# Kernel tuning notes

Hardware: AMD Instinct MI355X
Metric: run time of the kernel (lower is better)

The kernel has to match this reference:

```python
import jax, jax.numpy as jnp
import numpy as np

B, T, D, H = 128, 256, 1024, 1024


def setup_inputs() -> dict:
    key = jax.random.key(0)
    ks = jax.random.split(key, 6)
    s = 0.02
    return {
        "x": jax.random.normal(ks[0], (B, T, D), dtype=jnp.float32),
        "mask": jnp.ones((B, T), dtype=jnp.float32),
        "Wi_f": jax.random.normal(ks[1], (3 * H, D), dtype=jnp.float32) * s,
        "Wh_f": jax.random.normal(ks[2], (3 * H, H), dtype=jnp.float32) * s,
        "bi_f": jnp.zeros((3 * H,), dtype=jnp.float32),
        "bh_f": jnp.zeros((3 * H,), dtype=jnp.float32),
        "Wi_r": jax.random.normal(ks[3], (3 * H, D), dtype=jnp.float32) * s,
        "Wh_r": jax.random.normal(ks[4], (3 * H, H), dtype=jnp.float32) * s,
        "bi_r": jnp.zeros((3 * H,), dtype=jnp.float32),
        "bh_r": jnp.zeros((3 * H,), dtype=jnp.float32),
    }


def _gru_scan(x_tbd, m_tb, Wi, Wh, bi, bh):
    # x_tbd: [T,B,D], m_tb: [T,B]; returns all hidden states [T,B,H]
    h0 = jnp.zeros((x_tbd.shape[1], Wh.shape[1]), dtype=x_tbd.dtype)

    def step(h, inp):
        x_t, m_t = inp
        gi = x_t @ Wi.T + bi          # [B,3H]
        gh = h @ Wh.T + bh            # [B,3H]
        i_r, i_z, i_n = jnp.split(gi, 3, axis=-1)
        h_r, h_z, h_n = jnp.split(gh, 3, axis=-1)
        r = jax.nn.sigmoid(i_r + h_r)
        z = jax.nn.sigmoid(i_z + h_z)
        n = jnp.tanh(i_n + r * h_n)
        h_new = (1.0 - z) * n + z * h
        m = m_t[:, None]
        h_out = m * h_new + (1.0 - m) * h  # masked carry-over
        return h_out, h_out

    _, hs = jax.lax.scan(step, h0, (x_tbd, m_tb))
    return hs


def reference(x, mask, Wi_f, Wh_f, bi_f, bh_f, Wi_r, Wh_r, bi_r, bh_r):
    x_t = jnp.transpose(x, (1, 0, 2))   # [T,B,D]
    m_t = jnp.transpose(mask, (1, 0))   # [T,B]
    hs_f = _gru_scan(x_t, m_t, Wi_f, Wh_f, bi_f, bh_f)              # forward in time
    hs_r = _gru_scan(x_t[::-1], m_t[::-1], Wi_r, Wh_r, bi_r, bh_r)  # reverse in time
    hs_r = hs_r[::-1]
    out = jnp.concatenate([hs_f, hs_r], axis=-1)  # [T,B,2H]
    return jnp.transpose(out, (1, 0, 2))          # [B,T,2H]
```

## Files before the change

kernel.cpp:

```cpp
#include <hip/hip_runtime.h>
#include <hip/hip_bf16.h>

typedef __hip_bfloat16 bf16;
typedef __attribute__((ext_vector_type(8))) short bf16x8;
typedef __attribute__((ext_vector_type(4))) float f32x4;

#define GLDS16(g, l)                                                  \
  __builtin_amdgcn_global_load_lds(                                   \
      (const __attribute__((address_space(1))) void*)(g),             \
      (__attribute__((address_space(3))) void*)(l), 16, 0, 0)

__device__ __forceinline__ float bf2f(bf16 v) { return __bfloat162float(v); }
__device__ __forceinline__ short f2bf(float f) {
  bf16 b = __float2bfloat16(f);
  return *reinterpret_cast<short*>(&b);
}

__device__ __forceinline__ unsigned long long ald64(const void* p) {
  return __hip_atomic_load((const unsigned long long*)p, __ATOMIC_RELAXED,
                           __HIP_MEMORY_SCOPE_AGENT);
}
__device__ __forceinline__ void ast32(void* p, unsigned v) {
  __hip_atomic_store((unsigned*)p, v, __ATOMIC_RELAXED,
                     __HIP_MEMORY_SCOPE_AGENT);
}
__device__ __forceinline__ unsigned ald32(const void* p) {
  return __hip_atomic_load((const unsigned*)p, __ATOMIC_RELAXED,
                           __HIP_MEMORY_SCOPE_AGENT);
}

__global__ __launch_bounds__(256) void cvt_bf16(const float* __restrict__ in,
                                                bf16* __restrict__ out, int n) {
  const int i = (blockIdx.x * 256 + threadIdx.x) * 8;
  if (i >= n) return;
  const float4 u = *(const float4*)(in + i);
  const float4 v = *(const float4*)(in + i + 4);
  bf16x8 w;
  w[0] = f2bf(u.x); w[1] = f2bf(u.y); w[2] = f2bf(u.z); w[3] = f2bf(u.w);
  w[4] = f2bf(v.x); w[5] = f2bf(v.y); w[6] = f2bf(v.z); w[7] = f2bf(v.w);
  *(bf16x8*)(out + i) = w;
}

__global__ __launch_bounds__(256) void cvt_whb(const float* __restrict__ Wh_f,
                                               const float* __restrict__ Wh_r,
                                               bf16* __restrict__ Whb) {
  const int t = blockIdx.x * 256 + threadIdx.x;
  const int d = t / 393216;
  int r = t % 393216;
  const int cg = r / 6144;  r %= 6144;
  const int g = r / 2048;   r %= 2048;
  const int kk = r / 64;
  const int lane = r & 63;
  const float* Wh = d ? Wh_r : Wh_f;
  const int row = g * 1024 + cg * 16 + (lane & 15);
  const int col = kk * 32 + (lane >> 4) * 8;
  const float* s = Wh + (size_t)row * 1024 + col;
  const float4 u = *(const float4*)s;
  const float4 v = *(const float4*)(s + 4);
  bf16x8 w;
  w[0] = f2bf(u.x); w[1] = f2bf(u.y); w[2] = f2bf(u.z); w[3] = f2bf(u.w);
  w[4] = f2bf(v.x); w[5] = f2bf(v.y); w[6] = f2bf(v.z); w[7] = f2bf(v.w);
  *(bf16x8*)(Whb + (size_t)t * 8) = w;
}

__global__ __launch_bounds__(256) void gi_gemm(const bf16* __restrict__ X,
                                               const bf16* __restrict__ Wi,
                                               const float* __restrict__ bi,
                                               bf16* __restrict__ Gi) {
  __shared__ bf16 As[128 * 32];
  __shared__ bf16 Bs[128 * 32];
  const int tid = threadIdx.x;
  const int lane = tid & 63;
  const int w = tid >> 6;
  const int wm = w >> 1, wn = w & 1;
  const int m0 = blockIdx.y * 128;
  const int n0 = blockIdx.x * 128;
  const int rA = lane & 15;
  const int kl = (lane >> 4) * 8;

  f32x4 acc[4][4] = {};

  const bf16* Ab = X + (size_t)m0 * 1024;
  const bf16* Bb = Wi + (size_t)n0 * 1024;

  const int arow = tid >> 2;
  const int akk = (tid & 3) * 8;

  for (int kt = 0; kt < 1024; kt += 32) {
#pragma unroll
    for (int i = 0; i < 2; ++i) {
      GLDS16(Ab + (size_t)(i * 64 + arow) * 1024 + kt + akk,
             As + (i * 256 + w * 64) * 8);
      GLDS16(Bb + (size_t)(i * 64 + arow) * 1024 + kt + akk,
             Bs + (i * 256 + w * 64) * 8);
    }
    asm volatile("s_waitcnt vmcnt(0)" ::: "memory");
    __syncthreads();

    bf16x8 a[4], b[4];
#pragma unroll
    for (int f = 0; f < 4; ++f) {
      a[f] = *(const bf16x8*)(As + (wm * 64 + f * 16 + rA) * 32 + kl);
      b[f] = *(const bf16x8*)(Bs + (wn * 64 + f * 16 + rA) * 32 + kl);
    }
#pragma unroll
    for (int mf = 0; mf < 4; ++mf)
#pragma unroll
      for (int nf = 0; nf < 4; ++nf)
        acc[mf][nf] = __builtin_amdgcn_mfma_f32_16x16x32_bf16(
            a[mf], b[nf], acc[mf][nf], 0, 0, 0);
    __syncthreads();
  }

  const int rgrp = (lane >> 4) * 4;
#pragma unroll
  for (int nf = 0; nf < 4; ++nf) {
    const int col = n0 + wn * 64 + nf * 16 + rA;
    const float bv = bi[col];
#pragma unroll
    for (int mf = 0; mf < 4; ++mf) {
#pragma unroll
      for (int j = 0; j < 4; ++j) {
        const int row = m0 + wm * 64 + mf * 16 + rgrp + j;
        Gi[(size_t)row * 3072 + col] = __float2bfloat16(acc[mf][nf][j] + bv);
      }
    }
  }
}

__global__ __launch_bounds__(128, 1) void gru_persist_f(
    const bf16* __restrict__ Whb, const float* __restrict__ bh_f,
    const float* __restrict__ bh_r, const bf16* __restrict__ Gi,
    const float* __restrict__ mask, bf16* __restrict__ h16,
    unsigned* __restrict__ flags, float* __restrict__ out) {
  __shared__ bf16 hs[32 * 1024];
  const int tid = threadIdx.x;
  const int lane = tid & 63;
  const int w = tid >> 6;
  const int mg = w;
  const int bid = blockIdx.x;
  const int chain = bid & 7;
  const int ct = bid >> 3;
  const int dir = chain >> 2;
  const int bt = chain & 3;
  unsigned* gflags = flags + chain * 128;

  const float* bh = dir ? bh_r : bh_f;
  const bf16* gi = Gi + (size_t)dir * (32768ull * 3072ull);
  const int bt0 = bt * 32;
  const int rA = lane & 15;
  const int klane = lane >> 4;
  const int row = mg * 16 + rA;
  const int colg = ct * 16 + rA;

  bf16* hbuf0 = h16 + (size_t)(dir * 2 + 0) * 131072;
  bf16* hbuf1 = h16 + (size_t)(dir * 2 + 1) * 131072;

  const bf16* bp = Whb + (size_t)dir * 3145728 + (size_t)(ct * 3) * 16384 +
                   lane * 8;
  bf16x8 br[32], bz[32];
#pragma unroll
  for (int kk = 0; kk < 32; ++kk) br[kk] = *(const bf16x8*)(bp + kk * 512);
#pragma unroll
  for (int kk = 0; kk < 32; ++kk)
    bz[kk] = *(const bf16x8*)(bp + 16384 + kk * 512);
  const bf16* bpn = bp + 32768;

  const float bhr = bh[colg];
  const float bhz = bh[1024 + colg];
  const float bhn = bh[2048 + colg];

  float hp[4] = {0.f, 0.f, 0.f, 0.f};
  const int brow0 = bt0 + mg * 16 + klane * 4;

  float gir[4], giz[4], gin[4], mk4[4];
  {
    const int time0 = dir ? 255 : 0;
#pragma unroll
    for (int j = 0; j < 4; ++j) {
      const size_t gbase = ((size_t)(brow0 + j) * 256 + time0) * 3072 + colg;
      gir[j] = bf2f(gi[gbase]);
      giz[j] = bf2f(gi[gbase + 1024]);
      gin[j] = bf2f(gi[gbase + 2048]);
      mk4[j] = mask[(brow0 + j) * 256 + time0];
    }
  }

  for (int t = 0; t < 256; ++t) {
    const int time = dir ? (255 - t) : t;
    bf16* hin = (t & 1) ? hbuf1 : hbuf0;
    bf16* hout = (t & 1) ? hbuf0 : hbuf1;

#pragma unroll
    for (int b4 = 0; b4 < 4; ++b4) {
      unsigned long long vv[16];
#pragma unroll
      for (int q = 0; q < 16; ++q) {
        const int idx = (b4 * 16 + q) * 128 + tid;
        const int r = idx >> 8;
        const int c8 = idx & 255;
        vv[q] = ald64(hin + ((size_t)(bt0 + r) << 10) + c8 * 4);
      }
#pragma unroll
      for (int q = 0; q < 16; ++q) {
        const int idx = (b4 * 16 + q) * 128 + tid;
        const int r = idx >> 8;
        const int c8 = idx & 255;
        const int sw = (((c8 >> 1) ^ (r & 7)) << 4) | ((c8 & 1) << 3);
        *(unsigned long long*)((char*)hs + r * 2048 + sw) = vv[q];
      }
    }
    __syncthreads();

    f32x4 acc0 = {}, acc1 = {}, acc2 = {};
#pragma unroll
    for (int kk = 0; kk < 32; ++kk) {
      const int cidx = kk * 4 + klane;
      bf16x8 a = *(const bf16x8*)(hs + row * 1024 + ((cidx ^ (row & 7)) << 3));
      bf16x8 bn = *(const bf16x8*)(bpn + kk * 512);
      acc0 = __builtin_amdgcn_mfma_f32_16x16x32_bf16(a, br[kk], acc0, 0, 0, 0);
      acc1 = __builtin_amdgcn_mfma_f32_16x16x32_bf16(a, bz[kk], acc1, 0, 0, 0);
      acc2 = __builtin_amdgcn_mfma_f32_16x16x32_bf16(a, bn, acc2, 0, 0, 0);
    }

    float hnv[4];
#pragma unroll
    for (int j = 0; j < 4; ++j) {
      const float gr = acc0[j] + bhr + gir[j];
      const float gz = acc1[j] + bhz + giz[j];
      const float ghn = acc2[j] + bhn;
      const float r = 1.f / (1.f + __expf(-gr));
      const float z = 1.f / (1.f + __expf(-gz));
      const float nin = gin[j] + r * ghn;
      const float n = 1.f - 2.f / (__expf(2.f * nin) + 1.f);
      float hn = (1.f - z) * n + z * hp[j];
      hn = mk4[j] * hn + (1.f - mk4[j]) * hp[j];
      hp[j] = hn;
      hnv[j] = hn;
      const unsigned short hb = (unsigned short)f2bf(hn);
      const unsigned nb = (unsigned)__shfl_xor((int)hb, 1);
      if (!(lane & 1))
        ast32(hout + (((size_t)brow0 + j) << 10) + colg,
              (unsigned)hb | (nb << 16));
    }

    asm volatile("s_waitcnt vmcnt(0)" ::: "memory");
    __syncthreads();
    if (tid == 0) ast32(&gflags[ct], (unsigned)(t + 1));

#pragma unroll
    for (int j = 0; j < 4; ++j)
      out[(((size_t)(brow0 + j)) * 256 + time) * 2048 + (size_t)(dir * 1024) +
          colg] = hnv[j];

    if (t < 255) {
      const int tn = dir ? (254 - t) : (t + 1);
#pragma unroll
      for (int j = 0; j < 4; ++j) {
        const size_t gbase = ((size_t)(brow0 + j) * 256 + tn) * 3072 + colg;
        gir[j] = bf2f(gi[gbase]);
        giz[j] = bf2f(gi[gbase + 1024]);
        gin[j] = bf2f(gi[gbase + 2048]);
        mk4[j] = mask[(brow0 + j) * 256 + tn];
      }
      if (w == 0) {
        unsigned v;
        do {
          __builtin_amdgcn_s_sleep(1);
          v = ald32(&gflags[lane]);
        } while (__any((int)(v < (unsigned)(t + 1))));
      }
      __builtin_amdgcn_sched_barrier(0);
      __syncthreads();
    }
  }
}

__global__ __launch_bounds__(256, 1) void gru_persist_s(
    const bf16* __restrict__ Whb, const float* __restrict__ bh_f,
    const float* __restrict__ bh_r, const bf16* __restrict__ Gi,
    const float* __restrict__ mask, bf16* __restrict__ h16,
    unsigned* __restrict__ flags, float* __restrict__ out) {
  __shared__ bf16 hs[32 * 1024];
  const int tid = threadIdx.x;
  const int lane = tid & 63;
  const int w = tid >> 6;
  const int mg = w >> 1;
  const int cg = w & 1;
  const int ct = blockIdx.x;
  const int bt = blockIdx.y;
  const int dir = blockIdx.z;
  unsigned* gflags = flags + (dir * 4 + bt) * 128;

  const float* bh = dir ? bh_r : bh_f;
  const bf16* gi = Gi + (size_t)dir * (32768ull * 3072ull);
  const int bt0 = bt * 32;
  const int rA = lane & 15;
  const int klane = lane >> 4;
  const int row = mg * 16 + rA;
  const int colg = ct * 32 + cg * 16 + rA;

  bf16* hbuf0 = h16 + (size_t)(dir * 2 + 0) * 131072;
  bf16* hbuf1 = h16 + (size_t)(dir * 2 + 1) * 131072;

  const bf16* bp = Whb + (size_t)dir * 3145728 +
                   (size_t)((ct * 2 + cg) * 3) * 16384 + lane * 8;
  bf16x8 br[32], bz[32];
#pragma unroll
  for (int kk = 0; kk < 32; ++kk) br[kk] = *(const bf16x8*)(bp + kk * 512);
#pragma unroll
  for (int kk = 0; kk < 32; ++kk)
    bz[kk] = *(const bf16x8*)(bp + 16384 + kk * 512);
  const bf16* bpn = bp + 32768;

  const float bhr = bh[colg];
  const float bhz = bh[1024 + colg];
  const float bhn = bh[2048 + colg];

  float hp[4] = {0.f, 0.f, 0.f, 0.f};
  const int brow0 = bt0 + mg * 16 + klane * 4;

  float gir[4], giz[4], gin[4], mk4[4];
  {
    const int time0 = dir ? 255 : 0;
#pragma unroll
    for (int j = 0; j < 4; ++j) {
      const size_t gbase = ((size_t)(brow0 + j) * 256 + time0) * 3072 + colg;
      gir[j] = bf2f(gi[gbase]);
      giz[j] = bf2f(gi[gbase + 1024]);
      gin[j] = bf2f(gi[gbase + 2048]);
      mk4[j] = mask[(brow0 + j) * 256 + time0];
    }
  }

  for (int t = 0; t < 256; ++t) {
    const int time = dir ? (255 - t) : t;
    bf16* hin = (t & 1) ? hbuf1 : hbuf0;
    bf16* hout = (t & 1) ? hbuf0 : hbuf1;

#pragma unroll
    for (int half = 0; half < 2; ++half) {
      unsigned long long vv[16];
#pragma unroll
      for (int q = 0; q < 16; ++q) {
        const int idx = (half * 16 + q) * 256 + tid;
        const int r = idx >> 8;
        const int c8 = idx & 255;
        vv[q] = ald64(hin + ((size_t)(bt0 + r) << 10) + c8 * 4);
      }
#pragma unroll
      for (int q = 0; q < 16; ++q) {
        const int idx = (half * 16 + q) * 256 + tid;
        const int r = idx >> 8;
        const int c8 = idx & 255;
        const int sw = (((c8 >> 1) ^ (r & 7)) << 4) | ((c8 & 1) << 3);
        *(unsigned long long*)((char*)hs + r * 2048 + sw) = vv[q];
      }
    }
    __syncthreads();

    f32x4 acc0 = {}, acc1 = {}, acc2 = {};
#pragma unroll
    for (int kk = 0; kk < 32; ++kk) {
      const int cidx = kk * 4 + klane;
      bf16x8 a = *(const bf16x8*)(hs + row * 1024 + ((cidx ^ (row & 7)) << 3));
      bf16x8 bn = *(const bf16x8*)(bpn + kk * 512);
      acc0 = __builtin_amdgcn_mfma_f32_16x16x32_bf16(a, br[kk], acc0, 0, 0, 0);
      acc1 = __builtin_amdgcn_mfma_f32_16x16x32_bf16(a, bz[kk], acc1, 0, 0, 0);
      acc2 = __builtin_amdgcn_mfma_f32_16x16x32_bf16(a, bn, acc2, 0, 0, 0);
    }

    float hnv[4];
#pragma unroll
    for (int j = 0; j < 4; ++j) {
      const float gr = acc0[j] + bhr + gir[j];
      const float gz = acc1[j] + bhz + giz[j];
      const float ghn = acc2[j] + bhn;
      const float r = 1.f / (1.f + __expf(-gr));
      const float z = 1.f / (1.f + __expf(-gz));
      const float nin = gin[j] + r * ghn;
      const float n = 1.f - 2.f / (__expf(2.f * nin) + 1.f);
      float hn = (1.f - z) * n + z * hp[j];
      hn = mk4[j] * hn + (1.f - mk4[j]) * hp[j];
      hp[j] = hn;
      hnv[j] = hn;
      const unsigned short hb = (unsigned short)f2bf(hn);
      const unsigned nb = (unsigned)__shfl_xor((int)hb, 1);
      if (!(lane & 1))
        ast32(hout + (((size_t)brow0 + j) << 10) + colg,
              (unsigned)hb | (nb << 16));
    }

    asm volatile("s_waitcnt vmcnt(0)" ::: "memory");
    __syncthreads();
    if (tid == 0) ast32(&gflags[ct], (unsigned)(t + 1));

#pragma unroll
    for (int j = 0; j < 4; ++j)
      out[(((size_t)(brow0 + j)) * 256 + time) * 2048 + (size_t)(dir * 1024) +
          colg] = hnv[j];

    if (t < 255) {
      const int tn = dir ? (254 - t) : (t + 1);
#pragma unroll
      for (int j = 0; j < 4; ++j) {
        const size_t gbase = ((size_t)(brow0 + j) * 256 + tn) * 3072 + colg;
        gir[j] = bf2f(gi[gbase]);
        giz[j] = bf2f(gi[gbase + 1024]);
        gin[j] = bf2f(gi[gbase + 2048]);
        mk4[j] = mask[(brow0 + j) * 256 + tn];
      }
      if (w == 0) {
        unsigned v;
        do {
          __builtin_amdgcn_s_sleep(1);
          v = ald32(&gflags[lane & 31]);
        } while (__any((int)(v < (unsigned)(t + 1))));
      }
      __builtin_amdgcn_sched_barrier(0);
      __syncthreads();
    }
  }
}

extern "C" void kernel_launch(void* const* d_in, const int* in_sizes, int n_in,
                              void* d_out, int out_size, void* d_ws,
                              size_t ws_size, hipStream_t stream) {
  const float* x = (const float*)d_in[0];
  const float* mask = (const float*)d_in[1];
  const float* Wi_f = (const float*)d_in[2];
  const float* Wh_f = (const float*)d_in[3];
  const float* bi_f = (const float*)d_in[4];
  const float* bh_f = (const float*)d_in[5];
  const float* Wi_r = (const float*)d_in[6];
  const float* Wh_r = (const float*)d_in[7];
  const float* bi_r = (const float*)d_in[8];
  const float* bh_r = (const float*)d_in[9];
  float* out = (float*)d_out;

  char* ws = (char*)d_ws;
  const size_t GI_ELEMS = 32768ull * 3072ull;
  bf16* Gi = (bf16*)ws;
  bf16* Whb = (bf16*)(ws + 2 * GI_ELEMS * sizeof(bf16));
  bf16* h16 = Whb + 2 * 3145728;
  unsigned* flags = (unsigned*)((char*)h16 + 1048576);

  bf16* Xb = (bf16*)d_out;
  bf16* Wib_f = Xb + 33554432;
  bf16* Wib_r = Wib_f + 3145728;

  hipMemsetAsync(h16, 0, 1048576 + 4096, stream);

  cvt_bf16<<<16384, 256, 0, stream>>>(x, Xb, 33554432);
  cvt_bf16<<<1536, 256, 0, stream>>>(Wi_f, Wib_f, 3145728);
  cvt_bf16<<<1536, 256, 0, stream>>>(Wi_r, Wib_r, 3145728);
  cvt_whb<<<3072, 256, 0, stream>>>(Wh_f, Wh_r, Whb);

  gi_gemm<<<dim3(24, 256), 256, 0, stream>>>(Xb, Wib_f, bi_f, Gi);
  gi_gemm<<<dim3(24, 256), 256, 0, stream>>>(Xb, Wib_r, bi_r, Gi + GI_ELEMS);

  int occ = 0;
  (void)hipOccupancyMaxActiveBlocksPerMultiprocessor(&occ, gru_persist_f, 128,
                                                     0);
  if (occ >= 2)
    gru_persist_f<<<dim3(512), 128, 0, stream>>>(Whb, bh_f, bh_r, Gi, mask,
                                                 h16, flags, out);
  else
    gru_persist_s<<<dim3(32, 4, 2), 256, 0, stream>>>(Whb, bh_f, bh_r, Gi,
                                                      mask, h16, flags, out);
}
```

Measured before the change: 2.479 ms.

## Use per-timestep hidden-state ring buffer to drop double-buffer hazard and atomic loads

Adds a persistent GRU kernel that writes each timestep's bf16 hidden state into its own ring slot in workspace, so readers no longer race with writers of the next step. Blocks wait for the flag right before loading the previous step's state, and the loads become plain 16-byte vector loads instead of 8-byte relaxed atomic loads. The older 128-thread variant chosen by occupancy is removed. In exchange the ring needs a large workspace and runs only when ws_size allows, with the old double-buffer kernel kept as the fallback.

```diff
diff --git a/kernel.cpp b/kernel.cpp
--- a/kernel.cpp
+++ b/kernel.cpp
@@ -4,6 +4,7 @@
 typedef __hip_bfloat16 bf16;
 typedef __attribute__((ext_vector_type(8))) short bf16x8;
 typedef __attribute__((ext_vector_type(4))) float f32x4;
+typedef __attribute__((ext_vector_type(2))) unsigned long long u64x2;
 
 #define GLDS16(g, l)                                                  \
   __builtin_amdgcn_global_load_lds(                                   \
@@ -128,7 +129,157 @@
   }
 }
 
-__global__ __launch_bounds__(128, 1) void gru_persist_f(
+__global__ __launch_bounds__(256, 1) void gru_persist_r(
+    const bf16* __restrict__ Whb, const float* __restrict__ bh_f,
+    const float* __restrict__ bh_r, const bf16* __restrict__ Gi,
+    const float* __restrict__ mask, const bf16* __restrict__ zbuf,
+    bf16* __restrict__ ring, unsigned* __restrict__ flags,
+    float* __restrict__ out) {
+  __shared__ bf16 hs[32 * 1024];
+  const int tid = threadIdx.x;
+  const int lane = tid & 63;
+  const int w = tid >> 6;
+  const int mg = w >> 1;
+  const int cg = w & 1;
+  const int ct = blockIdx.x;
+  const int bt = blockIdx.y;
+  const int dir = blockIdx.z;
+  unsigned* gflags = flags + (dir * 4 + bt) * 128;
+
+  const float* bh = dir ? bh_r : bh_f;
+  const bf16* gi = Gi + (size_t)dir * (32768ull * 3072ull);
+  const int bt0 = bt * 32;
+  const int rA = lane & 15;
+  const int klane = lane >> 4;
+  const int row = mg * 16 + rA;
+  const int colg = ct * 32 + cg * 16 + rA;
+
+  const bf16* bp = Whb + (size_t)dir * 3145728 +
+                   (size_t)((ct * 2 + cg) * 3) * 16384 + lane * 8;
+  bf16x8 br[32], bz[32];
+#pragma unroll
+  for (int kk = 0; kk < 32; ++kk) br[kk] = *(const bf16x8*)(bp + kk * 512);
+#pragma unroll
+  for (int kk = 0; kk < 32; ++kk)
+    bz[kk] = *(const bf16x8*)(bp + 16384 + kk * 512);
+  const bf16* bpn = bp + 32768;
+
+  const float bhr = bh[colg];
+  const float bhz = bh[1024 + colg];
+  const float bhn = bh[2048 + colg];
+
+  float hp[4] = {0.f, 0.f, 0.f, 0.f};
+  const int brow0 = bt0 + mg * 16 + klane * 4;
+
+  float gir[4], giz[4], gin[4], mk4[4];
+  {
+    const int time0 = dir ? 255 : 0;
+#pragma unroll
+    for (int j = 0; j < 4; ++j) {
+      const size_t gbase = ((size_t)(brow0 + j) * 256 + time0) * 3072 + colg;
+      gir[j] = bf2f(gi[gbase]);
+      giz[j] = bf2f(gi[gbase + 1024]);
+      gin[j] = bf2f(gi[gbase + 2048]);
+      mk4[j] = mask[(brow0 + j) * 256 + time0];
+    }
+  }
+
+  for (int t = 0; t < 256; ++t) {
+    const int time = dir ? (255 - t) : t;
+
+    if (t > 0) {
+      if (w == 0) {
+        unsigned v;
+        do {
+          __builtin_amdgcn_s_sleep(1);
+          v = ald32(&gflags[lane & 31]);
+        } while (__any((int)(v < (unsigned)t)));
+      }
+      __builtin_amdgcn_sched_barrier(0);
+      __syncthreads();
+      asm volatile("" ::: "memory");
+    }
+
+    const bf16* hsrc =
+        (t == 0) ? (zbuf + (size_t)bt0 * 1024)
+                 : (ring + (size_t)(t - 1) * 262144 + (size_t)dir * 131072 +
+                    (size_t)bt0 * 1024);
+    {
+      u64x2 v[16];
+#pragma unroll
+      for (int q = 0; q < 16; ++q) {
+        const int idx = q * 256 + tid;
+        const int r = idx >> 7;
+        const int ch = idx & 127;
+        v[q] = *(const u64x2*)(hsrc + ((size_t)r << 10) + ch * 8);
+      }
+#pragma unroll
+      for (int q = 0; q < 16; ++q) {
+        const int idx = q * 256 + tid;
+        const int r = idx >> 7;
+        const int ch = idx & 127;
+        *(u64x2*)((char*)hs + r * 2048 + ((ch ^ (r & 7)) << 4)) = v[q];
+      }
+    }
+    __syncthreads();
+
+    f32x4 acc0 = {}, acc1 = {}, acc2 = {};
+#pragma unroll
+    for (int kk = 0; kk < 32; ++kk) {
+      const int cidx = kk * 4 + klane;
+      bf16x8 a = *(const bf16x8*)(hs + row * 1024 + ((cidx ^ (row & 7)) << 3));
+      bf16x8 bn = *(const bf16x8*)(bpn + kk * 512);
+      acc0 = __builtin_amdgcn_mfma_f32_16x16x32_bf16(a, br[kk], acc0, 0, 0, 0);
+      acc1 = __builtin_amdgcn_mfma_f32_16x16x32_bf16(a, bz[kk], acc1, 0, 0, 0);
+      acc2 = __builtin_amdgcn_mfma_f32_16x16x32_bf16(a, bn, acc2, 0, 0, 0);
+    }
+
+    bf16* hdst = ring + (size_t)t * 262144 + (size_t)dir * 131072;
+    float hnv[4];
+#pragma unroll
+    for (int j = 0; j < 4; ++j) {
+      const float gr = acc0[j] + bhr + gir[j];
+      const float gz = acc1[j] + bhz + giz[j];
+      const float ghn = acc2[j] + bhn;
+      const float r = 1.f / (1.f + __expf(-gr));
+      const float z = 1.f / (1.f + __expf(-gz));
+      const float nin = gin[j] + r * ghn;
+      const float n = 1.f - 2.f / (__expf(2.f * nin) + 1.f);
+      float hn = (1.f - z) * n + z * hp[j];
+      hn = mk4[j] * hn + (1.f - mk4[j]) * hp[j];
+      hp[j] = hn;
+      hnv[j] = hn;
+      const unsigned short hb = (unsigned short)f2bf(hn);
+      const unsigned nb = (unsigned)__shfl_xor((int)hb, 1);
+      if (!(lane & 1))
+        ast32(hdst + (((size_t)brow0 + j) << 10) + colg,
+              (unsigned)hb | (nb << 16));
+    }
+
+    asm volatile("s_waitcnt vmcnt(0)" ::: "memory");
+    __syncthreads();
+    if (tid == 0) ast32(&gflags[ct], (unsigned)(t + 1));
+
+#pragma unroll
+    for (int j = 0; j < 4; ++j)
+      out[(((size_t)(brow0 + j)) * 256 + time) * 2048 + (size_t)(dir * 1024) +
+          colg] = hnv[j];
+
+    if (t < 255) {
+      const int tn = dir ? (254 - t) : (t + 1);
+#pragma unroll
+      for (int j = 0; j < 4; ++j) {
+        const size_t gbase = ((size_t)(brow0 + j) * 256 + tn) * 3072 + colg;
+        gir[j] = bf2f(gi[gbase]);
+        giz[j] = bf2f(gi[gbase + 1024]);
+        gin[j] = bf2f(gi[gbase + 2048]);
+        mk4[j] = mask[(brow0 + j) * 256 + tn];
+      }
+    }
+  }
+}
+
+__global__ __launch_bounds__(256, 1) void gru_persist_s(
     const bf16* __restrict__ Whb, const float* __restrict__ bh_f,
     const float* __restrict__ bh_r, const bf16* __restrict__ Gi,
     const float* __restrict__ mask, bf16* __restrict__ h16,
@@ -137,13 +288,12 @@
   const int tid = threadIdx.x;
   const int lane = tid & 63;
   const int w = tid >> 6;
-  const int mg = w;
-  const int bid = blockIdx.x;
-  const int chain = bid & 7;
-  const int ct = bid >> 3;
-  const int dir = chain >> 2;
-  const int bt = chain & 3;
-  unsigned* gflags = flags + chain * 128;
+  const int mg = w >> 1;
+  const int cg = w & 1;
+  const int ct = blockIdx.x;
+  const int bt = blockIdx.y;
+  const int dir = blockIdx.z;
+  unsigned* gflags = flags + (dir * 4 + bt) * 128;
 
   const float* bh = dir ? bh_r : bh_f;
   const bf16* gi = Gi + (size_t)dir * (32768ull * 3072ull);
@@ -151,13 +301,13 @@
   const int rA = lane & 15;
   const int klane = lane >> 4;
   const int row = mg * 16 + rA;
-  const int colg = ct * 16 + rA;
+  const int colg = ct * 32 + cg * 16 + rA;
 
   bf16* hbuf0 = h16 + (size_t)(dir * 2 + 0) * 131072;
   bf16* hbuf1 = h16 + (size_t)(dir * 2 + 1) * 131072;
 
-  const bf16* bp = Whb + (size_t)dir * 3145728 + (size_t)(ct * 3) * 16384 +
-                   lane * 8;
+  const bf16* bp = Whb + (size_t)dir * 3145728 +
+                   (size_t)((ct * 2 + cg) * 3) * 16384 + lane * 8;
   bf16x8 br[32], bz[32];
 #pragma unroll
   for (int kk = 0; kk < 32; ++kk) br[kk] = *(const bf16x8*)(bp + kk * 512);
@@ -192,18 +342,18 @@
     bf16* hout = (t & 1) ? hbuf0 : hbuf1;
 
 #pragma unroll
-    for (int b4 = 0; b4 < 4; ++b4) {
+    for (int half = 0; half < 2; ++half) {
       unsigned long long vv[16];
 #pragma unroll
       for (int q = 0; q < 16; ++q) {
-        const int idx = (b4 * 16 + q) * 128 + tid;
+        const int idx = (half * 16 + q) * 256 + tid;
         const int r = idx >> 8;
         const int c8 = idx & 255;
         vv[q] = ald64(hin + ((size_t)(bt0 + r) << 10) + c8 * 4);
       }
 #pragma unroll
       for (int q = 0; q < 16; ++q) {
-        const int idx = (b4 * 16 + q) * 128 + tid;
+        const int idx = (half * 16 + q) * 256 + tid;
         const int r = idx >> 8;
         const int c8 = idx & 255;
         const int sw = (((c8 >> 1) ^ (r & 7)) << 4) | ((c8 & 1) << 3);
@@ -267,153 +417,6 @@
         unsigned v;
         do {
           __builtin_amdgcn_s_sleep(1);
-          v = ald32(&gflags[lane]);
-        } while (__any((int)(v < (unsigned)(t + 1))));
-      }
-      __builtin_amdgcn_sched_barrier(0);
-      __syncthreads();
-    }
-  }
-}
-
-__global__ __launch_bounds__(256, 1) void gru_persist_s(
-    const bf16* __restrict__ Whb, const float* __restrict__ bh_f,
-    const float* __restrict__ bh_r, const bf16* __restrict__ Gi,
-    const float* __restrict__ mask, bf16* __restrict__ h16,
-    unsigned* __restrict__ flags, float* __restrict__ out) {
-  __shared__ bf16 hs[32 * 1024];
-  const int tid = threadIdx.x;
-  const int lane = tid & 63;
-  const int w = tid >> 6;
-  const int mg = w >> 1;
-  const int cg = w & 1;
-  const int ct = blockIdx.x;
-  const int bt = blockIdx.y;
-  const int dir = blockIdx.z;
-  unsigned* gflags = flags + (dir * 4 + bt) * 128;
-
-  const float* bh = dir ? bh_r : bh_f;
-  const bf16* gi = Gi + (size_t)dir * (32768ull * 3072ull);
-  const int bt0 = bt * 32;
-  const int rA = lane & 15;
-  const int klane = lane >> 4;
-  const int row = mg * 16 + rA;
-  const int colg = ct * 32 + cg * 16 + rA;
-
-  bf16* hbuf0 = h16 + (size_t)(dir * 2 + 0) * 131072;
-  bf16* hbuf1 = h16 + (size_t)(dir * 2 + 1) * 131072;
-
-  const bf16* bp = Whb + (size_t)dir * 3145728 +
-                   (size_t)((ct * 2 + cg) * 3) * 16384 + lane * 8;
-  bf16x8 br[32], bz[32];
-#pragma unroll
-  for (int kk = 0; kk < 32; ++kk) br[kk] = *(const bf16x8*)(bp + kk * 512);
-#pragma unroll
-  for (int kk = 0; kk < 32; ++kk)
-    bz[kk] = *(const bf16x8*)(bp + 16384 + kk * 512);
-  const bf16* bpn = bp + 32768;
-
-  const float bhr = bh[colg];
-  const float bhz = bh[1024 + colg];
-  const float bhn = bh[2048 + colg];
-
-  float hp[4] = {0.f, 0.f, 0.f, 0.f};
-  const int brow0 = bt0 + mg * 16 + klane * 4;
-
-  float gir[4], giz[4], gin[4], mk4[4];
-  {
-    const int time0 = dir ? 255 : 0;
-#pragma unroll
-    for (int j = 0; j < 4; ++j) {
-      const size_t gbase = ((size_t)(brow0 + j) * 256 + time0) * 3072 + colg;
-      gir[j] = bf2f(gi[gbase]);
-      giz[j] = bf2f(gi[gbase + 1024]);
-      gin[j] = bf2f(gi[gbase + 2048]);
-      mk4[j] = mask[(brow0 + j) * 256 + time0];
-    }
-  }
-
-  for (int t = 0; t < 256; ++t) {
-    const int time = dir ? (255 - t) : t;
-    bf16* hin = (t & 1) ? hbuf1 : hbuf0;
-    bf16* hout = (t & 1) ? hbuf0 : hbuf1;
-
-#pragma unroll
-    for (int half = 0; half < 2; ++half) {
-      unsigned long long vv[16];
-#pragma unroll
-      for (int q = 0; q < 16; ++q) {
-        const int idx = (half * 16 + q) * 256 + tid;
-        const int r = idx >> 8;
-        const int c8 = idx & 255;
-        vv[q] = ald64(hin + ((size_t)(bt0 + r) << 10) + c8 * 4);
-      }
-#pragma unroll
-      for (int q = 0; q < 16; ++q) {
-        const int idx = (half * 16 + q) * 256 + tid;
-        const int r = idx >> 8;
-        const int c8 = idx & 255;
-        const int sw = (((c8 >> 1) ^ (r & 7)) << 4) | ((c8 & 1) << 3);
-        *(unsigned long long*)((char*)hs + r * 2048 + sw) = vv[q];
-      }
-    }
-    __syncthreads();
-
-    f32x4 acc0 = {}, acc1 = {}, acc2 = {};
-#pragma unroll
-    for (int kk = 0; kk < 32; ++kk) {
-      const int cidx = kk * 4 + klane;
-      bf16x8 a = *(const bf16x8*)(hs + row * 1024 + ((cidx ^ (row & 7)) << 3));
-      bf16x8 bn = *(const bf16x8*)(bpn + kk * 512);
-      acc0 = __builtin_amdgcn_mfma_f32_16x16x32_bf16(a, br[kk], acc0, 0, 0, 0);
-      acc1 = __builtin_amdgcn_mfma_f32_16x16x32_bf16(a, bz[kk], acc1, 0, 0, 0);
-      acc2 = __builtin_amdgcn_mfma_f32_16x16x32_bf16(a, bn, acc2, 0, 0, 0);
-    }
-
-    float hnv[4];
-#pragma unroll
-    for (int j = 0; j < 4; ++j) {
-      const float gr = acc0[j] + bhr + gir[j];
-      const float gz = acc1[j] + bhz + giz[j];
-      const float ghn = acc2[j] + bhn;
-      const float r = 1.f / (1.f + __expf(-gr));
-      const float z = 1.f / (1.f + __expf(-gz));
-      const float nin = gin[j] + r * ghn;
-      const float n = 1.f - 2.f / (__expf(2.f * nin) + 1.f);
-      float hn = (1.f - z) * n + z * hp[j];
-      hn = mk4[j] * hn + (1.f - mk4[j]) * hp[j];
-      hp[j] = hn;
-      hnv[j] = hn;
-      const unsigned short hb = (unsigned short)f2bf(hn);
-      const unsigned nb = (unsigned)__shfl_xor((int)hb, 1);
-      if (!(lane & 1))
-        ast32(hout + (((size_t)brow0 + j) << 10) + colg,
-              (unsigned)hb | (nb << 16));
-    }
-
-    asm volatile("s_waitcnt vmcnt(0)" ::: "memory");
-    __syncthreads();
-    if (tid == 0) ast32(&gflags[ct], (unsigned)(t + 1));
-
-#pragma unroll
-    for (int j = 0; j < 4; ++j)
-      out[(((size_t)(brow0 + j)) * 256 + time) * 2048 + (size_t)(dir * 1024) +
-          colg] = hnv[j];
-
-    if (t < 255) {
-      const int tn = dir ? (254 - t) : (t + 1);
-#pragma unroll
-      for (int j = 0; j < 4; ++j) {
-        const size_t gbase = ((size_t)(brow0 + j) * 256 + tn) * 3072 + colg;
-        gir[j] = bf2f(gi[gbase]);
-        giz[j] = bf2f(gi[gbase + 1024]);
-        gin[j] = bf2f(gi[gbase + 2048]);
-        mk4[j] = mask[(brow0 + j) * 256 + tn];
-      }
-      if (w == 0) {
-        unsigned v;
-        do {
-          __builtin_amdgcn_s_sleep(1);
           v = ald32(&gflags[lane & 31]);
         } while (__any((int)(v < (unsigned)(t + 1))));
       }
@@ -444,12 +447,17 @@
   bf16* Whb = (bf16*)(ws + 2 * GI_ELEMS * sizeof(bf16));
   bf16* h16 = Whb + 2 * 3145728;
   unsigned* flags = (unsigned*)((char*)h16 + 1048576);
+  bf16* zbuf = (bf16*)((char*)flags + 4096);
+  bf16* ring = (bf16*)((char*)zbuf + 262144);
+  const size_t ring_end =
+      (size_t)((char*)ring - ws) + 256ull * 262144ull * sizeof(bf16);
+  const bool use_ring = ws_size >= ring_end;
 
   bf16* Xb = (bf16*)d_out;
   bf16* Wib_f = Xb + 33554432;
   bf16* Wib_r = Wib_f + 3145728;
 
-  hipMemsetAsync(h16, 0, 1048576 + 4096, stream);
+  hipMemsetAsync(h16, 0, 1048576 + 4096 + 262144, stream);
 
   cvt_bf16<<<16384, 256, 0, stream>>>(x, Xb, 33554432);
   cvt_bf16<<<1536, 256, 0, stream>>>(Wi_f, Wib_f, 3145728);
@@ -459,12 +467,9 @@
   gi_gemm<<<dim3(24, 256), 256, 0, stream>>>(Xb, Wib_f, bi_f, Gi);
   gi_gemm<<<dim3(24, 256), 256, 0, stream>>>(Xb, Wib_r, bi_r, Gi + GI_ELEMS);
 
-  int occ = 0;
-  (void)hipOccupancyMaxActiveBlocksPerMultiprocessor(&occ, gru_persist_f, 128,
-                                                     0);
-  if (occ >= 2)
-    gru_persist_f<<<dim3(512), 128, 0, stream>>>(Whb, bh_f, bh_r, Gi, mask,
-                                                 h16, flags, out);
+  if (use_ring)
+    gru_persist_r<<<dim3(32, 4, 2), 256, 0, stream>>>(
+        Whb, bh_f, bh_r, Gi, mask, zbuf, ring, flags, out);
   else
     gru_persist_s<<<dim3(32, 4, 2), 256, 0, stream>>>(Whb, bh_f, bh_r, Gi,
                                                       mask, h16, flags, out);
```

Measured after the change: 4.098 ms. 65.3% more time.
